# Optimization experiments

Measured on AMD Instinct MI355X. Metric: run time of the kernel, lower is better.

Reference implementation:

```python
import jax, jax.numpy as jnp
import numpy as np

B, H, W, N, DIM = 2, 64, 64, 4, 128
HEADS = 4
SPLIT = 2          # split_size; idx == 0 -> window = (H, SPLIT)
HEAD_DIM = DIM // HEADS
SCALE = HEAD_DIM ** -0.5


def setup_inputs() -> dict:
    key = jax.random.key(0)
    k1, k2, k3, k4 = jax.random.split(key, 4)
    query = jax.random.normal(k1, (B, H, W, N, DIM), jnp.float32)
    key_t = jax.random.normal(k2, (B, H, W, N, DIM), jnp.float32)
    value = jax.random.normal(k3, (B, H, W, N, DIM), jnp.float32)
    conv_w = jax.random.normal(k4, (DIM, 1, 3, 3), jnp.float32) * 0.1  # depthwise get_v
    return {"query": query, "key": key_t, "value": value, "conv_w": conv_w}


def _im2cswin(x, hs, ws, heads):
    # b (i hs) (j ws) n (h d) -> (b i j) h (hs ws n) d
    b, ht, wd, n, c = x.shape
    i, j = ht // hs, wd // ws
    d = c // heads
    x = x.reshape(b, i, hs, j, ws, n, heads, d)
    x = x.transpose(0, 1, 3, 6, 2, 4, 5, 7)  # b i j h hs ws n d
    return x.reshape(b * i * j, heads, hs * ws * n, d)


def _cswin_forward(query, key, value, conv_w):
    b, ht, wd, n, c = query.shape
    hs, ws = ht, SPLIT  # idx == 0; ht % hs == 0 and wd % ws == 0 -> no padding
    i, j = ht // hs, wd // ws
    Bw = b * i * j

    q = _im2cswin(query, hs, ws, HEADS) * SCALE
    k = _im2cswin(key, hs, ws, HEADS)

    # --- get_rpe (locally-enhanced positional encoding on value) ---
    # value windows: b i j n c hs ws
    vw = value.reshape(b, i, hs, j, ws, n, c).transpose(0, 1, 3, 5, 6, 2, 4)
    vw = vw.reshape(Bw, n, c, hs, ws)
    vimg = vw.reshape(Bw * n, c, hs, ws)
    conv = jax.lax.conv_general_dilated(
        vimg, conv_w, window_strides=(1, 1), padding=((1, 1), (1, 1)),
        dimension_numbers=("NCHW", "OIHW", "NCHW"), feature_group_count=c)
    conv = conv.reshape(Bw, n, c, hs, ws)
    rpe = conv.sum(axis=1, keepdims=True)  # Bw 1 c hs ws
    # subtract center-tap contribution of all other candidates at same pixel
    mask_n = (1.0 - jnp.eye(n, dtype=query.dtype)) * -1.0  # (n, n)
    center = conv_w[:, 0, 1, 1]  # (c,)
    tmp = vw * center[None, None, :, None, None]
    tmp = jnp.einsum("jk,bkdhw->bjdhw", mask_n, tmp)
    rpe = rpe + tmp  # Bw n c hs ws

    def to_tokens(t):
        # b n (h d) hs ws -> b h (hs ws n) d
        t = t.reshape(Bw, n, HEADS, HEAD_DIM, hs, ws)
        t = t.transpose(0, 2, 4, 5, 1, 3)
        return t.reshape(Bw, HEADS, hs * ws * n, HEAD_DIM)

    rpe = to_tokens(rpe)
    v = to_tokens(vw)

    # --- window attention mask: block self-edges between candidates at same pixel ---
    L = hs * ws * n
    tok = jnp.arange(L)
    sp = tok // n  # spatial index of each token
    amask = jnp.where(sp[:, None] == sp[None, :], -jnp.inf, 0.0)
    amask = jnp.where(tok[:, None] == tok[None, :], 0.0, amask).astype(query.dtype)

    attn = jnp.einsum("bhic,bhjc->bhij", q, k) + amask[None, None]
    attn = jax.nn.softmax(attn, axis=-1)
    x = jnp.einsum("bhij,bhjc->bhic", attn, v) + rpe

    # (b i j) h (hs ws n) d -> b (i hs) (j ws) n (h d)
    x = x.reshape(b, i, j, HEADS, hs, ws, n, HEAD_DIM)
    x = x.transpose(0, 1, 4, 2, 5, 6, 3, 7).reshape(b, ht, wd, n, c)
    return x


def reference(query, key, value, conv_w):
    return _cswin_forward(query, key, value, conv_w)
```

## Files before the change

kernel.cpp:

```cpp
#include <hip/hip_runtime.h>
#include <stdint.h>


typedef __bf16 bf16x8 __attribute__((ext_vector_type(8)));
typedef float f32x4 __attribute__((ext_vector_type(4)));
typedef float f32x2 __attribute__((ext_vector_type(2)));

#if __has_builtin(__builtin_amdgcn_exp2f)
#define EXP2F __builtin_amdgcn_exp2f
#else
#define EXP2F exp2f
#endif

union U4 { uint4 u; bf16x8 v; unsigned short s[8]; };

__device__ __forceinline__ float bf2f(unsigned short h){ union{unsigned u;float f;}x; x.u=((unsigned)h)<<16; return x.f; }

__device__ __forceinline__ unsigned cvtpk(float lo, float hi){
  unsigned d;
  asm("v_cvt_pk_bf16_f32 %0, %1, %2" : "=v"(d) : "v"(lo), "v"(hi));
  return d;
}
__device__ __forceinline__ U4 pack8(float4 a, float4 b){
  U4 r;
  r.u.x = cvtpk(a.x, a.y); r.u.y = cvtpk(a.z, a.w);
  r.u.z = cvtpk(b.x, b.y); r.u.w = cvtpk(b.z, b.w);
  return r;
}

__device__ __forceinline__ void pls32(unsigned &a, unsigned &b){
#if __has_builtin(__builtin_amdgcn_permlane32_swap)
  auto r = __builtin_amdgcn_permlane32_swap(a, b, false, false);
  a = r[0]; b = r[1];
#else
  unsigned sa_ = __shfl_xor(a, 32), sb_ = __shfl_xor(b, 32);
  bool hi = ((threadIdx.x & 32) != 0);
  unsigned na = hi ? sb_ : a, nb = hi ? b : sa_;
  a = na; b = nb;
#endif
}
__device__ __forceinline__ void pls16(unsigned &a, unsigned &b){
#if __has_builtin(__builtin_amdgcn_permlane16_swap)
  auto r = __builtin_amdgcn_permlane16_swap(a, b, false, false);
  a = r[0]; b = r[1];
#else
  unsigned sa_ = __shfl_xor(a, 16), sb_ = __shfl_xor(b, 16);
  bool hi = ((threadIdx.x & 16) != 0);
  unsigned na = hi ? sb_ : a, nb = hi ? b : sa_;
  a = na; b = nb;
#endif
}

__device__ __forceinline__ void xpose_p(const unsigned w[4][2], U4& ap0, U4& ap1)
{
  unsigned a0 = w[0][0], b0 = w[1][0]; pls32(a0, b0); pls16(a0, b0);
  unsigned a1 = w[0][1], b1 = w[1][1]; pls32(a1, b1); pls16(a1, b1);
  ap0.u.x = a0; ap0.u.y = a1; ap0.u.z = b0; ap0.u.w = b1;
  unsigned c0 = w[2][0], d0 = w[3][0]; pls32(c0, d0); pls16(c0, d0);
  unsigned c1 = w[2][1], d1 = w[3][1]; pls32(c1, d1); pls16(c1, d1);
  ap1.u.x = c0; ap1.u.y = c1; ap1.u.z = d0; ap1.u.w = d1;
}

#define C_SCALE 0.25506953149031837f
#define M_SHIFT 20.0f

#define VT_OFF 0
#define KS_OFF 32768
#define LDS_BYTES 65536

__global__ __launch_bounds__(256, 2) void cswin_attn_kernel(
    const float* __restrict__ qg,
    const float* __restrict__ kg,
    const float* __restrict__ vg,
    const float* __restrict__ cwg,
    float* __restrict__ outg)
{
  __shared__ __align__(16) unsigned char smem[LDS_BYTES];
  const int tid = threadIdx.x;
  const int lane = tid & 63;
  const int wave = tid >> 6;
  const int qd = lane >> 4;
  const int n  = lane & 15;

  const int swn = (n & 7) << 2;
  const int xb0 = ((4 * qd) ^ swn) << 2;
  const int xb1 = xb0 ^ 64;

  const int bid = blockIdx.x;
  const int bh = ((bid >> 5) << 3) | (bid & 7);
  const int q4 = (bid >> 3) & 3;
  const int head = bh & 3;
  const int bw = bh >> 2;
  const int b  = bw >> 5;
  const int jj = bw & 31;

  const size_t wbase = (size_t)b * 2097152 + (size_t)(jj * 2) * 512 + head * 32;
  const size_t lane_base = wbase + (size_t)(n >> 3) * 32768 + (size_t)((n >> 2) & 1) * 512 +
                           (size_t)(n & 3) * 128 + qd * 8;

  const int row0  = q4 * 128 + wave * 32;
  const int tilea = row0 >> 4;
  const int cka   = tilea >> 2;
  const int ta    = tilea & 3;

  float4 qra0, qra1, qrb0, qrb1;
  {
    const float* qa = qg + lane_base + (size_t)tilea * 65536;
    const float* qb = qa + 65536;
    qra0 = ((const float4*)qa)[0]; qra1 = ((const float4*)qa)[1];
    qrb0 = ((const float4*)qb)[0]; qrb1 = ((const float4*)qb)[1];
  }

  {
    const int tk = tid >> 3;
    const int p  = tid & 7;
#pragma unroll 1
    for (int rr = 0; rr < 2; rr++){
      float4 va[8], ka[8];
#pragma unroll
      for (int r = 0; r < 8; r++){
        int T = (rr * 8 + r) * 32 + tk;
        size_t toff = wbase + (size_t)(T >> 3) * 32768 + (size_t)((T >> 2) & 1) * 512 +
                      (size_t)(T & 3) * 128 + p * 4;
        va[r] = *(const float4*)(vg + toff);
        ka[r] = *(const float4*)(kg + toff);
      }
#pragma unroll
      for (int r = 0; r < 8; r++){
        int T = (rr * 8 + r) * 32 + tk;
        unsigned short h0 = (unsigned short)cvtpk(va[r].x, va[r].x);
        unsigned short h1 = (unsigned short)cvtpk(va[r].y, va[r].y);
        unsigned short h2 = (unsigned short)cvtpk(va[r].z, va[r].z);
        unsigned short h3 = (unsigned short)cvtpk(va[r].w, va[r].w);
        int R0 = 4 * p;
        *(unsigned short*)(smem + VT_OFF + (R0+0) * 1024 + ((T*2) ^ (((R0+0)&7)<<4))) = h0;
        *(unsigned short*)(smem + VT_OFF + (R0+1) * 1024 + ((T*2) ^ (((R0+1)&7)<<4))) = h1;
        *(unsigned short*)(smem + VT_OFF + (R0+2) * 1024 + ((T*2) ^ (((R0+2)&7)<<4))) = h2;
        *(unsigned short*)(smem + VT_OFF + (R0+3) * 1024 + ((T*2) ^ (((R0+3)&7)<<4))) = h3;
        uint2 kw; kw.x = cvtpk(ka[r].x, ka[r].y); kw.y = cvtpk(ka[r].z, ka[r].w);
        *(uint2*)(smem + KS_OFF + T * 64 + ((p*8) ^ ((T&3)<<4))) = kw;
      }
    }
  }

  __syncthreads();

  U4 bqa = pack8(qra0, qra1);
  U4 bqb = pack8(qrb0, qrb1);

  f32x4 o0a={0,0,0,0}, o1a={0,0,0,0}, o0b={0,0,0,0}, o1b={0,0,0,0};
  f32x2 la2 = {0.f,0.f}, lb2 = {0.f,0.f};

  const int kxb = (qd * 16) ^ ((n & 3) << 4);
  const unsigned char* kbase = smem + KS_OFF + n * 64 + kxb;

#pragma unroll 1
  for (int ck = 0; ck < 8; ck++){
    U4 ak[4];
    const unsigned char* kb = kbase + ck * 4096;
    ak[0].u = *(const uint4*)(kb);
    ak[1].u = *(const uint4*)(kb + 1024);
    ak[2].u = *(const uint4*)(kb + 2048);
    ak[3].u = *(const uint4*)(kb + 3072);

    const f32x4 zero = {0.f,0.f,0.f,0.f};
    f32x4 sa[4], sb[4];
#pragma unroll
    for (int t = 0; t < 4; t++){
      sa[t] = __builtin_amdgcn_mfma_f32_16x16x32_bf16(ak[t].v, bqa.v, zero, 0, 0, 0);
      sb[t] = __builtin_amdgcn_mfma_f32_16x16x32_bf16(ak[t].v, bqb.v, zero, 0, 0, 0);
    }
    if (ck == cka){
      bool dq = (qd == (n >> 2));
#pragma unroll
      for (int r = 0; r < 4; r++)
        if (dq && r != (n & 3)){ sa[ta][r] = -1e30f; sb[ta+1][r] = -1e30f; }
    }

    unsigned wA[4][2], wB[4][2];
    {
      const f32x2 m2 = {-M_SHIFT, -M_SHIFT};
#pragma unroll
      for (int t = 0; t < 4; t++){
        f32x2 y0 = (f32x2){sa[t][0], sa[t][1]} * C_SCALE + m2;
        f32x2 y1 = (f32x2){sa[t][2], sa[t][3]} * C_SCALE + m2;
        float p0 = EXP2F(y0.x), p1 = EXP2F(y0.y);
        float p2 = EXP2F(y1.x), p3 = EXP2F(y1.y);
        la2 += (f32x2){p0, p1}; la2 += (f32x2){p2, p3};
        wA[t][0] = cvtpk(p0, p1); wA[t][1] = cvtpk(p2, p3);
      }
#pragma unroll
      for (int t = 0; t < 4; t++){
        f32x2 y0 = (f32x2){sb[t][0], sb[t][1]} * C_SCALE + m2;
        f32x2 y1 = (f32x2){sb[t][2], sb[t][3]} * C_SCALE + m2;
        float p0 = EXP2F(y0.x), p1 = EXP2F(y0.y);
        float p2 = EXP2F(y1.x), p3 = EXP2F(y1.y);
        lb2 += (f32x2){p0, p1}; lb2 += (f32x2){p2, p3};
        wB[t][0] = cvtpk(p0, p1); wB[t][1] = cvtpk(p2, p3);
      }
    }

    const unsigned char* vr0 = smem + VT_OFF + n * 1024 + ck * 128;
    const unsigned char* vr1 = vr0 + 16 * 1024;
    U4 bv00, bv01, bv10, bv11;
    bv00.u = *(const uint4*)(vr0 + xb0);
    bv01.u = *(const uint4*)(vr0 + xb1);
    bv10.u = *(const uint4*)(vr1 + xb0);
    bv11.u = *(const uint4*)(vr1 + xb1);

    U4 apA0, apA1, apB0, apB1;
    xpose_p(wA, apA0, apA1);
    xpose_p(wB, apB0, apB1);

    o0a = __builtin_amdgcn_mfma_f32_16x16x32_bf16(apA0.v, bv00.v, o0a, 0, 0, 0);
    o0a = __builtin_amdgcn_mfma_f32_16x16x32_bf16(apA1.v, bv01.v, o0a, 0, 0, 0);
    o1a = __builtin_amdgcn_mfma_f32_16x16x32_bf16(apA0.v, bv10.v, o1a, 0, 0, 0);
    o1a = __builtin_amdgcn_mfma_f32_16x16x32_bf16(apA1.v, bv11.v, o1a, 0, 0, 0);
    o0b = __builtin_amdgcn_mfma_f32_16x16x32_bf16(apB0.v, bv00.v, o0b, 0, 0, 0);
    o0b = __builtin_amdgcn_mfma_f32_16x16x32_bf16(apB1.v, bv01.v, o0b, 0, 0, 0);
    o1b = __builtin_amdgcn_mfma_f32_16x16x32_bf16(apB0.v, bv10.v, o1b, 0, 0, 0);
    o1b = __builtin_amdgcn_mfma_f32_16x16x32_bf16(apB1.v, bv11.v, o1b, 0, 0, 0);
  }

  float w9[2][9];
#pragma unroll
  for (int nt = 0; nt < 2; nt++){
    int c = head * 32 + nt * 16 + n;
#pragma unroll
    for (int t9 = 0; t9 < 9; t9++) w9[nt][t9] = cwg[c * 9 + t9];
  }

  float la = la2.x + la2.y, lb = lb2.x + lb2.y;
  la += __shfl_xor(la, 16); la += __shfl_xor(la, 32);
  lb += __shfl_xor(lb, 16); lb += __shfl_xor(lb, 32);

  const float ila = 1.f / la, ilb = 1.f / lb;

#pragma unroll
  for (int mt = 0; mt < 2; mt++){
    const int m0 = row0 + mt * 16;
    const float ilv = mt ? ilb : ila;
    const f32x4 oo0 = mt ? o0b : o0a;
    const f32x4 oo1 = mt ? o1b : o1a;
    float il[4];
#pragma unroll
    for (int r = 0; r < 4; r++) il[r] = __shfl(ilv, qd * 4 + r);

    const int sp = (m0 >> 2) + qd;
    const int h_ = sp >> 1, w_ = sp & 1;

    float accs[2], cw2[2], vfs[2][4];
#pragma unroll
    for (int nt = 0; nt < 2; nt++){
      const int d = nt * 16 + n;
      const unsigned char* VTd = smem + VT_OFF + d * 1024;
      float acc = 0.f;
#pragma unroll
      for (int dy = -1; dy <= 1; dy++){
        int h2 = h_ + dy;
        bool hv = (h2 >= 0) && (h2 <= 63);
        int h2c = hv ? h2 : h_;
#pragma unroll
        for (int wp = 0; wp < 2; wp++){
          bool valid = hv && !((dy == 0) && (wp == w_));
          int ti = (dy + 1) * 3 + 1 + wp - w_;
          int spn = h2c * 2 + wp;
          uint2 sv = *(const uint2*)(VTd + (((2 * spn) ^ swn) << 2));
          float s = bf2f((unsigned short)(sv.x & 0xffff)) + bf2f((unsigned short)(sv.x >> 16))
                  + bf2f((unsigned short)(sv.y & 0xffff)) + bf2f((unsigned short)(sv.y >> 16));
          acc += (valid ? w9[nt][ti] : 0.f) * s;
        }
      }
      accs[nt] = acc;
      cw2[nt] = w9[nt][4];
      uint2 vv4 = *(const uint2*)(VTd + ((((m0 >> 1) + 2 * qd) ^ swn) << 2));
      vfs[nt][0] = bf2f((unsigned short)(vv4.x & 0xffff));
      vfs[nt][1] = bf2f((unsigned short)(vv4.x >> 16));
      vfs[nt][2] = bf2f((unsigned short)(vv4.y & 0xffff));
      vfs[nt][3] = bf2f((unsigned short)(vv4.y >> 16));
    }

    const size_t obase = (size_t)b * 2097152 + (size_t)h_ * 32768 +
                         (size_t)(jj * 2 + w_) * 512 + head * 32;
#pragma unroll
    for (int r = 0; r < 4; r++){
      float r0 = oo0[r] * il[r] + accs[0] + cw2[0] * vfs[0][r];
      float r1 = oo1[r] * il[r] + accs[1] + cw2[1] * vfs[1][r];
      outg[obase + (size_t)r * 128 + n]      = r0;
      outg[obase + (size_t)r * 128 + 16 + n] = r1;
    }
  }
}

extern "C" void kernel_launch(void* const* d_in, const int* in_sizes, int n_in,
                              void* d_out, int out_size, void* d_ws, size_t ws_size,
                              hipStream_t stream) {
  (void)in_sizes; (void)n_in; (void)d_ws; (void)ws_size; (void)out_size;
  cswin_attn_kernel<<<dim3(1024), dim3(256), 0, stream>>>(
      (const float*)d_in[0], (const float*)d_in[1], (const float*)d_in[2],
      (const float*)d_in[3], (float*)d_out);
}
```

Before: 117.9 us.

## Merge four query-quarter blocks into one 1024-thread block per window-head

Each window-head is now handled by a single 1024-thread block covering all query rows, instead of four 256-thread blocks that each reloaded and converted the full K/V tile into LDS. This removes the redundant global loads and bf16 conversion of K and V across the four blocks. The K-tile LDS swizzle also changes from (T&3) to ((T>>1)&3), with the matching read index, to alter the bank-conflict pattern. In exchange the grid shrinks to 256 blocks with one block per CU, so occupancy and latency hiding drop, and the new swizzle's correctness depends on the reads and writes staying consistent.

```diff
diff --git a/kernel.cpp b/kernel.cpp
--- a/kernel.cpp
+++ b/kernel.cpp
@@ -68,7 +68,7 @@
 #define KS_OFF 32768
 #define LDS_BYTES 65536
 
-__global__ __launch_bounds__(256, 2) void cswin_attn_kernel(
+__global__ __launch_bounds__(1024, 1) void cswin_attn_kernel(
     const float* __restrict__ qg,
     const float* __restrict__ kg,
     const float* __restrict__ vg,
@@ -86,9 +86,7 @@
   const int xb0 = ((4 * qd) ^ swn) << 2;
   const int xb1 = xb0 ^ 64;
 
-  const int bid = blockIdx.x;
-  const int bh = ((bid >> 5) << 3) | (bid & 7);
-  const int q4 = (bid >> 3) & 3;
+  const int bh = blockIdx.x;
   const int head = bh & 3;
   const int bw = bh >> 2;
   const int b  = bw >> 5;
@@ -98,7 +96,7 @@
   const size_t lane_base = wbase + (size_t)(n >> 3) * 32768 + (size_t)((n >> 2) & 1) * 512 +
                            (size_t)(n & 3) * 128 + qd * 8;
 
-  const int row0  = q4 * 128 + wave * 32;
+  const int row0  = wave * 32;
   const int tilea = row0 >> 4;
   const int cka   = tilea >> 2;
   const int ta    = tilea & 3;
@@ -114,33 +112,37 @@
   {
     const int tk = tid >> 3;
     const int p  = tid & 7;
-#pragma unroll 1
-    for (int rr = 0; rr < 2; rr++){
-      float4 va[8], ka[8];
-#pragma unroll
-      for (int r = 0; r < 8; r++){
-        int T = (rr * 8 + r) * 32 + tk;
-        size_t toff = wbase + (size_t)(T >> 3) * 32768 + (size_t)((T >> 2) & 1) * 512 +
-                      (size_t)(T & 3) * 128 + p * 4;
-        va[r] = *(const float4*)(vg + toff);
-        ka[r] = *(const float4*)(kg + toff);
-      }
-#pragma unroll
-      for (int r = 0; r < 8; r++){
-        int T = (rr * 8 + r) * 32 + tk;
-        unsigned short h0 = (unsigned short)cvtpk(va[r].x, va[r].x);
-        unsigned short h1 = (unsigned short)cvtpk(va[r].y, va[r].y);
-        unsigned short h2 = (unsigned short)cvtpk(va[r].z, va[r].z);
-        unsigned short h3 = (unsigned short)cvtpk(va[r].w, va[r].w);
-        int R0 = 4 * p;
-        *(unsigned short*)(smem + VT_OFF + (R0+0) * 1024 + ((T*2) ^ (((R0+0)&7)<<4))) = h0;
-        *(unsigned short*)(smem + VT_OFF + (R0+1) * 1024 + ((T*2) ^ (((R0+1)&7)<<4))) = h1;
-        *(unsigned short*)(smem + VT_OFF + (R0+2) * 1024 + ((T*2) ^ (((R0+2)&7)<<4))) = h2;
-        *(unsigned short*)(smem + VT_OFF + (R0+3) * 1024 + ((T*2) ^ (((R0+3)&7)<<4))) = h3;
-        uint2 kw; kw.x = cvtpk(ka[r].x, ka[r].y); kw.y = cvtpk(ka[r].z, ka[r].w);
-        *(uint2*)(smem + KS_OFF + T * 64 + ((p*8) ^ ((T&3)<<4))) = kw;
-      }
-    }
+    float4 va0, va1, va2, va3, ka0, ka1, ka2, ka3;
+    {
+      size_t o0 = wbase + (size_t)((tk) >> 3) * 32768 + (size_t)(((tk) >> 2) & 1) * 512 + (size_t)((tk) & 3) * 128 + p * 4;
+      size_t o1 = wbase + (size_t)((128 + tk) >> 3) * 32768 + (size_t)(((128 + tk) >> 2) & 1) * 512 + (size_t)((128 + tk) & 3) * 128 + p * 4;
+      size_t o2 = wbase + (size_t)((256 + tk) >> 3) * 32768 + (size_t)(((256 + tk) >> 2) & 1) * 512 + (size_t)((256 + tk) & 3) * 128 + p * 4;
+      size_t o3 = wbase + (size_t)((384 + tk) >> 3) * 32768 + (size_t)(((384 + tk) >> 2) & 1) * 512 + (size_t)((384 + tk) & 3) * 128 + p * 4;
+      va0 = *(const float4*)(vg + o0); ka0 = *(const float4*)(kg + o0);
+      va1 = *(const float4*)(vg + o1); ka1 = *(const float4*)(kg + o1);
+      va2 = *(const float4*)(vg + o2); ka2 = *(const float4*)(kg + o2);
+      va3 = *(const float4*)(vg + o3); ka3 = *(const float4*)(kg + o3);
+    }
+    const int R0 = 4 * p;
+#define STAGE_WR(VA, KA, TT)                                                         \
+    {                                                                                \
+      const int T_ = (TT);                                                           \
+      unsigned short h0 = (unsigned short)cvtpk((VA).x, (VA).x);                     \
+      unsigned short h1 = (unsigned short)cvtpk((VA).y, (VA).y);                     \
+      unsigned short h2 = (unsigned short)cvtpk((VA).z, (VA).z);                     \
+      unsigned short h3 = (unsigned short)cvtpk((VA).w, (VA).w);                     \
+      *(unsigned short*)(smem + VT_OFF + (R0+0) * 1024 + ((T_*2) ^ (((R0+0)&7)<<4))) = h0; \
+      *(unsigned short*)(smem + VT_OFF + (R0+1) * 1024 + ((T_*2) ^ (((R0+1)&7)<<4))) = h1; \
+      *(unsigned short*)(smem + VT_OFF + (R0+2) * 1024 + ((T_*2) ^ (((R0+2)&7)<<4))) = h2; \
+      *(unsigned short*)(smem + VT_OFF + (R0+3) * 1024 + ((T_*2) ^ (((R0+3)&7)<<4))) = h3; \
+      uint2 kw; kw.x = cvtpk((KA).x, (KA).y); kw.y = cvtpk((KA).z, (KA).w);          \
+      *(uint2*)(smem + KS_OFF + T_ * 64 + ((p*8) ^ (((T_>>1)&3)<<4))) = kw;          \
+    }
+    STAGE_WR(va0, ka0, tk)
+    STAGE_WR(va1, ka1, 128 + tk)
+    STAGE_WR(va2, ka2, 256 + tk)
+    STAGE_WR(va3, ka3, 384 + tk)
+#undef STAGE_WR
   }
 
   __syncthreads();
@@ -151,7 +153,7 @@
   f32x4 o0a={0,0,0,0}, o1a={0,0,0,0}, o0b={0,0,0,0}, o1b={0,0,0,0};
   f32x2 la2 = {0.f,0.f}, lb2 = {0.f,0.f};
 
-  const int kxb = (qd * 16) ^ ((n & 3) << 4);
+  const int kxb = (qd * 16) ^ (((n >> 1) & 3) << 4);
   const unsigned char* kbase = smem + KS_OFF + n * 64 + kxb;
 
 #pragma unroll 1
@@ -296,7 +298,7 @@
                               void* d_out, int out_size, void* d_ws, size_t ws_size,
                               hipStream_t stream) {
   (void)in_sizes; (void)n_in; (void)d_ws; (void)ws_size; (void)out_size;
-  cswin_attn_kernel<<<dim3(1024), dim3(256), 0, stream>>>(
+  cswin_attn_kernel<<<dim3(256), dim3(1024), 0, stream>>>(
       (const float*)d_in[0], (const float*)d_in[1], (const float*)d_in[2],
       (const float*)d_in[3], (float*)d_out);
 }
```

Result: faster. 112.9 us (-4.3%).
